# Kernel tuning notes

Hardware: AMD Instinct MI355X
Metric: run time of the kernel (lower is better)

## Reference

```python
import math
import jax, jax.numpy as jnp
import numpy as np
from jax import lax

B, C, O, K, WDIM, H, W = 8, 512, 512, 3, 512, 64, 64
CONV_SCALE = 1.0 / math.sqrt(C * K * K)
MOD_SCALE = 1.0 / math.sqrt(WDIM)


def setup_inputs() -> dict:
    key = jax.random.key(0)
    k1, k2, k3, k4 = jax.random.split(key, 4)
    return {
        "x": jax.random.normal(k1, (B, C, H, W), dtype=jnp.float32),
        "w": jax.random.normal(k2, (B, WDIM), dtype=jnp.float32),
        "base_weight": jax.random.normal(k3, (1, O, C, K, K), dtype=jnp.float32),
        "mod_weight": jax.random.normal(k4, (C, WDIM), dtype=jnp.float32),
        "mod_bias": jnp.zeros((C,), dtype=jnp.float32),
    }


def reference(x, w, base_weight, mod_weight, mod_bias):
    # EqualLinear modulation: s in (B, C), then +1
    s = w @ (mod_weight * MOD_SCALE).T + mod_bias + 1.0  # (B, C)
    # Per-sample modulated weights: (B, O, C, K, K)
    weight = CONV_SCALE * base_weight * s[:, None, :, None, None]
    # Demodulation
    d = lax.rsqrt(jnp.sum(weight * weight, axis=(2, 3, 4), keepdims=True))
    weight = weight * d
    pad = K // 2

    def conv_one(xi, wi):
        # xi: (C, H, W), wi: (O, C, K, K)
        return lax.conv_general_dilated(
            xi[None], wi, window_strides=(1, 1),
            padding=[(pad, pad), (pad, pad)],
            dimension_numbers=("NCHW", "OIHW", "NCHW"),
        )[0]

    return jax.vmap(conv_one)(x, weight)  # (B, O, H, W)
```

## Files before the change

### kernel.cpp

```cpp
#include <hip/hip_runtime.h>
#include <stdint.h>


#define MOD_SCALE  0.044194173824159216f
#define CONV_SCALE 0.014731391274719739f

typedef __attribute__((ext_vector_type(4))) float f32x4;
typedef __attribute__((ext_vector_type(8))) short bf16x8;

__device__ inline unsigned short f2bf(float f) {
  uint32_t u = __float_as_uint(f);
  uint32_t r = (u + 0x7fffu + ((u >> 16) & 1u)) >> 16;
  return (unsigned short)r;
}

__device__ inline void gload_lds16(const void* g, void* l) {
  __builtin_amdgcn_global_load_lds(
      (const __attribute__((address_space(1))) void*)g,
      (__attribute__((address_space(3))) void*)l, 16, 0, 0);
}

__global__ __launch_bounds__(256) void k_style(const float* __restrict__ w,
                                               const float* __restrict__ modw,
                                               const float* __restrict__ modb,
                                               float* __restrict__ s_out) {
  __shared__ float red[256];
  const int tid = threadIdx.x;
  const int sb = blockIdx.x;
  const int cb = sb & 7, b = sb >> 3;
  const int cl = tid >> 2, qq = tid & 3;
  const int c = (cb << 6) + cl;
  const float4* wd = (const float4*)(w + (b << 9) + (qq << 7));
  const float4* md = (const float4*)(modw + ((size_t)c << 9) + (qq << 7));
  float acc = 0.f;
#pragma unroll
  for (int i = 0; i < 32; ++i) {
    float4 a = wd[i], m = md[i];
    acc += a.x * m.x + a.y * m.y + a.z * m.z + a.w * m.w;
  }
  red[tid] = acc;
  __syncthreads();
  if (tid < 64) {
    float v = red[tid * 4] + red[tid * 4 + 1] + red[tid * 4 + 2] + red[tid * 4 + 3];
    int cc = (cb << 6) + tid;
    s_out[(b << 9) + cc] = v * MOD_SCALE + modb[cc] + 1.0f;
  }
}

__global__ __launch_bounds__(256) void k_prep(const float* __restrict__ x,
                                              const float* __restrict__ s,
                                              unsigned short* __restrict__ xp) {
  __shared__ uint32_t tb[64 * 260];
  const int blk = blockIdx.x;
  const int tid = threadIdx.x;
  if (blk < 512) {
    const int b = blk >> 6, y = blk & 63;
    const int px4 = tid & 15;
    const int cp  = tid >> 4;
    const float* xb = x + (size_t)(b << 9) * 4096 + (y << 6) + (px4 << 2);
    const float* sb = s + (b << 9);
#pragma unroll
    for (int it = 0; it < 16; ++it) {
      const int cpair = cp + (it << 4);
      const int c0 = cpair << 1;
      const float4 a0 = *(const float4*)(xb + (size_t)c0 * 4096);
      const float4 a1 = *(const float4*)(xb + (size_t)(c0 + 1) * 4096);
      const float s0 = sb[c0], s1 = sb[c0 + 1];
      const int pxb = px4 << 2;
      tb[(pxb + 0) * 260 + cpair] = (uint32_t)f2bf(a0.x * s0) | ((uint32_t)f2bf(a1.x * s1) << 16);
      tb[(pxb + 1) * 260 + cpair] = (uint32_t)f2bf(a0.y * s0) | ((uint32_t)f2bf(a1.y * s1) << 16);
      tb[(pxb + 2) * 260 + cpair] = (uint32_t)f2bf(a0.z * s0) | ((uint32_t)f2bf(a1.z * s1) << 16);
      tb[(pxb + 3) * 260 + cpair] = (uint32_t)f2bf(a0.w * s0) | ((uint32_t)f2bf(a1.w * s1) << 16);
    }
    __syncthreads();
    const int wv = tid >> 6, l = tid & 63;
    uint32_t* xpw = (uint32_t*)xp;
#pragma unroll
    for (int it = 0; it < 16; ++it) {
      const int px = (wv << 4) + it;
      const uint4 v = *(const uint4*)(tb + px * 260 + (l << 2));
      const size_t base = ((size_t)b * 4356 + (size_t)(y + 1) * 66 + (px + 1)) << 8;
      ((uint4*)(xpw + base))[l] = v;
    }
  } else {
    const int q = blk - 512;
    const int b = q / 260, p = q - b * 260;
    int py, px;
    if (p < 66)       { py = 0;       px = p; }
    else if (p < 132) { py = 65;      px = p - 66; }
    else if (p < 196) { py = p - 131; px = 0; }
    else              { py = p - 195; px = 65; }
    uint32_t* dst = (uint32_t*)(xp + ((size_t)b * 4356 + py * 66 + px) * 512);
    dst[tid] = 0u;
  }
}

__global__ __launch_bounds__(256) void k_fwd(const float* __restrict__ bw,
                                             const float* __restrict__ s,
                                             unsigned short* __restrict__ awT,
                                             float* __restrict__ d_out) {
  __shared__ float lw[4608];
  __shared__ float ls[4096];
  __shared__ float red[32];
  const int tid = threadIdx.x;
  const int o = blockIdx.x;
  {
    const float4* src = (const float4*)(bw + (size_t)o * 4608);
    float4* dst = (float4*)lw;
#pragma unroll
    for (int i = 0; i < 4; ++i) dst[tid + (i << 8)] = src[tid + (i << 8)];
    if (tid < 128) dst[tid + 1024] = src[tid + 1024];
  }
  {
    const float4* src = (const float4*)s;
    float4* dst = (float4*)ls;
#pragma unroll
    for (int i = 0; i < 4; ++i) dst[tid + (i << 8)] = src[tid + (i << 8)];
  }
  __syncthreads();
  const int c0 = tid << 1;
  const int base = c0 * 9;
  float wq0 = 0.f, wq1 = 0.f;
#pragma unroll
  for (int j = 0; j < 9; ++j) {
    float a = lw[base + j];      wq0 += a * a;
    float b2 = lw[base + 9 + j]; wq1 += b2 * b2;
  }
  const int lane = tid & 63, wv = tid >> 6;
#pragma unroll
  for (int b = 0; b < 8; ++b) {
    float s0 = ls[(b << 9) + c0], s1 = ls[(b << 9) + c0 + 1];
    float v = wq0 * s0 * s0 + wq1 * s1 * s1;
#pragma unroll
    for (int off = 32; off > 0; off >>= 1) v += __shfl_down(v, off, 64);
    if (lane == 0) red[(b << 2) + wv] = v;
  }
  __syncthreads();
  if (tid < 8) {
    float a = red[tid << 2] + red[(tid << 2) + 1] + red[(tid << 2) + 2] + red[(tid << 2) + 3];
    d_out[(tid << 9) + o] = rsqrtf(a * (1.0f / 4608.0f)) * CONV_SCALE;
  }
  uint32_t* dst = (uint32_t*)(awT + (size_t)o * 4608);
#pragma unroll
  for (int j = 0; j < 9; ++j)
    dst[(j << 8) + tid] = (uint32_t)f2bf(lw[base + j]) |
                          ((uint32_t)f2bf(lw[base + 9 + j]) << 16);
}

__global__ __launch_bounds__(256, 4) void k_conv(const unsigned short* __restrict__ awT,
                                                 const unsigned short* __restrict__ xpad,
                                                 const float* __restrict__ dmod,
                                                 float* __restrict__ out) {
  __shared__ alignas(16) unsigned short As[3 * 4096];
  __shared__ alignas(16) unsigned short Bs[4224];
  const int tid = threadIdx.x;
  const int b  = blockIdx.z;
  const int m0 = blockIdx.y << 7;
  const int n0 = blockIdx.x << 7;
  const int y0 = n0 >> 6;

  const int srow4 = tid >> 2;
  const int sl    = ((tid & 3) - (tid >> 3)) & 3;
  const int scol  = sl << 3;

  const unsigned short* A0 = awT + (size_t)(m0 + srow4) * 4608 + scol;
  const unsigned short* B0 = xpad + (size_t)b * (66 * 66 * 512)
                                  + (size_t)(y0 * 66 + srow4) * 512 + scol;

  const int lane = tid & 63;
  const int wv   = tid >> 6;
  const int moff = (wv >> 1) << 6;
  const int noff = (wv & 1) << 6;
  const int noffp = noff ? 66 : 0;
  const int lm   = lane & 15;
  const int g4   = lane >> 4;

  const int arow = moff + lm;
  const int aoff = arow * 32 + (((g4 + (arow >> 1)) & 3) << 3);
  int boff[3];
#pragma unroll
  for (int kx = 0; kx < 3; ++kx) {
    const int rb = noffp + lm + kx;
    boff[kx] = rb * 32 + (((g4 + (rb >> 1)) & 3) << 3);
  }

  f32x4 acc[4][4];
#pragma unroll
  for (int i = 0; i < 4; ++i)
#pragma unroll
    for (int j = 0; j < 4; ++j) acc[i][j] = (f32x4){0.f, 0.f, 0.f, 0.f};

#pragma unroll 1
  for (int ky = 0; ky < 3; ++ky) {
#pragma unroll 1
    for (int kb = 0; kb < 16; ++kb) {
      const int kcol = kb << 5;
#pragma unroll
      for (int kx = 0; kx < 3; ++kx) {
        const unsigned short* Ap = A0 + ((ky * 3 + kx) << 9) + kcol;
#pragma unroll
        for (int g = 0; g < 2; ++g)
          gload_lds16(Ap + (size_t)(g << 6) * 4608,
                      As + (kx << 12) + (((g << 8) + tid) << 3));
      }
      const unsigned short* Bp = B0 + (size_t)(ky * 66) * 512 + kcol;
#pragma unroll
      for (int g = 0; g < 2; ++g)
        gload_lds16(Bp + (size_t)(g << 6) * 512, Bs + (((g << 8) + tid) << 3));
      if (tid < 16) gload_lds16(Bp + (size_t)128 * 512, Bs + ((512 + tid) << 3));
      __syncthreads();
      __builtin_amdgcn_s_setprio(1);
#pragma unroll
      for (int kx = 0; kx < 3; ++kx) {
        bf16x8 af[4], bf[4];
        const unsigned short* pa = As + (kx << 12) + aoff;
        const unsigned short* pb = Bs + boff[kx];
#pragma unroll
        for (int i = 0; i < 4; ++i) af[i] = *(const bf16x8*)(pa + (i << 9));
#pragma unroll
        for (int j = 0; j < 4; ++j) bf[j] = *(const bf16x8*)(pb + (j << 9));
#pragma unroll
        for (int i = 0; i < 4; ++i)
#pragma unroll
          for (int j = 0; j < 4; ++j)
            acc[i][j] = __builtin_amdgcn_mfma_f32_16x16x32_bf16(af[i], bf[j], acc[i][j], 0, 0, 0);
      }
      __builtin_amdgcn_s_setprio(0);
      __syncthreads();
    }
  }

  const float* dB = dmod + (b << 9) + m0 + moff;
  float* op = out + (size_t)((b << 9) + m0 + moff) * 4096 + n0 + noff;
#pragma unroll
  for (int i = 0; i < 4; ++i) {
#pragma unroll
    for (int r = 0; r < 4; ++r) {
      const int m = i * 16 + (g4 << 2) + r;
      const float dm = dB[m];
#pragma unroll
      for (int j = 0; j < 4; ++j)
        op[(size_t)m * 4096 + (j << 4) + lm] = acc[i][j][r] * dm;
    }
  }
}

extern "C" void kernel_launch(void* const* d_in, const int* in_sizes, int n_in,
                              void* d_out, int out_size, void* d_ws, size_t ws_size,
                              hipStream_t stream) {
  const float* x    = (const float*)d_in[0];
  const float* w    = (const float*)d_in[1];
  const float* bw   = (const float*)d_in[2];
  const float* modw = (const float*)d_in[3];
  const float* modb = (const float*)d_in[4];
  float* out = (float*)d_out;
  char* ws = (char*)d_ws;

  float* s_buf = (float*)(ws);
  float* d_buf = (float*)(ws + 16384);
  unsigned short* awT  = (unsigned short*)(ws + 32768);
  unsigned short* xpad = (unsigned short*)(ws + 4751360);

  (void)in_sizes; (void)n_in; (void)out_size; (void)ws_size;

  k_style<<<64,   256, 0, stream>>>(w, modw, modb, s_buf);
  k_fwd  <<<512,  256, 0, stream>>>(bw, s_buf, awT, d_buf);
  k_prep <<<2592, 256, 0, stream>>>(x, s_buf, xpad);
  k_conv <<<dim3(32, 4, 8), 256, 0, stream>>>(awT, xpad, d_buf, out);
}
```

Measured before the change: 280.5 us.

## Enlarge conv tile to 128x256 and remap block index for L2 locality

```diff
diff --git a/kernel.cpp b/kernel.cpp
--- a/kernel.cpp
+++ b/kernel.cpp
@@ -147,48 +147,55 @@
                           ((uint32_t)f2bf(lw[base + 9 + j]) << 16);
 }
 
-__global__ __launch_bounds__(256, 4) void k_conv(const unsigned short* __restrict__ awT,
+__global__ __launch_bounds__(256, 2) void k_conv(const unsigned short* __restrict__ awT,
                                                  const unsigned short* __restrict__ xpad,
                                                  const float* __restrict__ dmod,
                                                  float* __restrict__ out) {
   __shared__ alignas(16) unsigned short As[3 * 4096];
-  __shared__ alignas(16) unsigned short Bs[4224];
-  const int tid = threadIdx.x;
-  const int b  = blockIdx.z;
-  const int m0 = blockIdx.y << 7;
-  const int n0 = blockIdx.x << 7;
-  const int y0 = n0 >> 6;
+  __shared__ alignas(16) unsigned short Bs[8448];
+  const int tid = threadIdx.x;
+
+  const int bid = blockIdx.x;
+  const int g   = bid & 7;
+  const int k   = bid >> 3;
+  const int nI  = k & 15;
+  const int zq  = k >> 4;
+  const int b   = (zq << 1) | (g >> 2);
+  const int m0  = (g & 3) << 7;
+  const int n0  = nI << 8;
+  const int y0  = nI << 2;
 
   const int srow4 = tid >> 2;
   const int sl    = ((tid & 3) - (tid >> 3)) & 3;
   const int scol  = sl << 3;
 
   const unsigned short* A0 = awT + (size_t)(m0 + srow4) * 4608 + scol;
-  const unsigned short* B0 = xpad + (size_t)b * (66 * 66 * 512)
-                                  + (size_t)(y0 * 66 + srow4) * 512 + scol;
+  const size_t bx = (size_t)b * (66 * 66 * 512);
+  const unsigned short* B0 = xpad + bx + (size_t)(y0 * 66 + srow4) * 512 + scol;
 
   const int lane = tid & 63;
   const int wv   = tid >> 6;
   const int moff = (wv >> 1) << 6;
-  const int noff = (wv & 1) << 6;
-  const int noffp = noff ? 66 : 0;
+  const int noff2 = (wv & 1) << 1;
   const int lm   = lane & 15;
   const int g4   = lane >> 4;
 
   const int arow = moff + lm;
   const int aoff = arow * 32 + (((g4 + (arow >> 1)) & 3) << 3);
-  int boff[3];
-#pragma unroll
-  for (int kx = 0; kx < 3; ++kx) {
-    const int rb = noffp + lm + kx;
-    boff[kx] = rb * 32 + (((g4 + (rb >> 1)) & 3) << 3);
-  }
-
-  f32x4 acc[4][4];
+  int boff[3][2];
+#pragma unroll
+  for (int kx = 0; kx < 3; ++kx)
+#pragma unroll
+    for (int jc = 0; jc < 2; ++jc) {
+      const int rb = (noff2 + jc) * 66 + lm + kx;
+      boff[kx][jc] = rb * 32 + (((g4 + (rb >> 1)) & 3) << 3);
+    }
+
+  f32x4 acc[4][8];
 #pragma unroll
   for (int i = 0; i < 4; ++i)
 #pragma unroll
-    for (int j = 0; j < 4; ++j) acc[i][j] = (f32x4){0.f, 0.f, 0.f, 0.f};
+    for (int j = 0; j < 8; ++j) acc[i][j] = (f32x4){0.f, 0.f, 0.f, 0.f};
 
 #pragma unroll 1
   for (int ky = 0; ky < 3; ++ky) {
@@ -199,31 +206,35 @@
       for (int kx = 0; kx < 3; ++kx) {
         const unsigned short* Ap = A0 + ((ky * 3 + kx) << 9) + kcol;
 #pragma unroll
-        for (int g = 0; g < 2; ++g)
-          gload_lds16(Ap + (size_t)(g << 6) * 4608,
-                      As + (kx << 12) + (((g << 8) + tid) << 3));
+        for (int g2 = 0; g2 < 2; ++g2)
+          gload_lds16(Ap + (size_t)(g2 << 6) * 4608,
+                      As + (kx << 12) + (((g2 << 8) + tid) << 3));
       }
       const unsigned short* Bp = B0 + (size_t)(ky * 66) * 512 + kcol;
 #pragma unroll
-      for (int g = 0; g < 2; ++g)
-        gload_lds16(Bp + (size_t)(g << 6) * 512, Bs + (((g << 8) + tid) << 3));
-      if (tid < 16) gload_lds16(Bp + (size_t)128 * 512, Bs + ((512 + tid) << 3));
+      for (int g2 = 0; g2 < 4; ++g2)
+        gload_lds16(Bp + (size_t)(g2 << 6) * 512, Bs + (((g2 << 8) + tid) << 3));
+      if (tid < 32) gload_lds16(Bp + (size_t)256 * 512, Bs + ((1024 + tid) << 3));
       __syncthreads();
       __builtin_amdgcn_s_setprio(1);
 #pragma unroll
       for (int kx = 0; kx < 3; ++kx) {
-        bf16x8 af[4], bf[4];
+        bf16x8 af[4], bfr[8];
         const unsigned short* pa = As + (kx << 12) + aoff;
-        const unsigned short* pb = Bs + boff[kx];
 #pragma unroll
         for (int i = 0; i < 4; ++i) af[i] = *(const bf16x8*)(pa + (i << 9));
-#pragma unroll
-        for (int j = 0; j < 4; ++j) bf[j] = *(const bf16x8*)(pb + (j << 9));
+        const unsigned short* pb0 = Bs + boff[kx][0];
+        const unsigned short* pb1 = Bs + boff[kx][1];
+#pragma unroll
+        for (int j = 0; j < 4; ++j) {
+          bfr[j]     = *(const bf16x8*)(pb0 + (j << 9));
+          bfr[4 + j] = *(const bf16x8*)(pb1 + (j << 9));
+        }
 #pragma unroll
         for (int i = 0; i < 4; ++i)
 #pragma unroll
-          for (int j = 0; j < 4; ++j)
-            acc[i][j] = __builtin_amdgcn_mfma_f32_16x16x32_bf16(af[i], bf[j], acc[i][j], 0, 0, 0);
+          for (int j = 0; j < 8; ++j)
+            acc[i][j] = __builtin_amdgcn_mfma_f32_16x16x32_bf16(af[i], bfr[j], acc[i][j], 0, 0, 0);
       }
       __builtin_amdgcn_s_setprio(0);
       __syncthreads();
@@ -231,7 +242,7 @@
   }
 
   const float* dB = dmod + (b << 9) + m0 + moff;
-  float* op = out + (size_t)((b << 9) + m0 + moff) * 4096 + n0 + noff;
+  float* op = out + (size_t)((b << 9) + m0 + moff) * 4096 + n0 + ((wv & 1) << 7);
 #pragma unroll
   for (int i = 0; i < 4; ++i) {
 #pragma unroll
@@ -239,7 +250,7 @@
       const int m = i * 16 + (g4 << 2) + r;
       const float dm = dB[m];
 #pragma unroll
-      for (int j = 0; j < 4; ++j)
+      for (int j = 0; j < 8; ++j)
         op[(size_t)m * 4096 + (j << 4) + lm] = acc[i][j][r] * dm;
     }
   }
@@ -266,5 +277,5 @@
   k_style<<<64,   256, 0, stream>>>(w, modw, modb, s_buf);
   k_fwd  <<<512,  256, 0, stream>>>(bw, s_buf, awT, d_buf);
   k_prep <<<2592, 256, 0, stream>>>(x, s_buf, xpad);
-  k_conv <<<dim3(32, 4, 8), 256, 0, stream>>>(awT, xpad, d_buf, out);
-}
+  k_conv <<<512,  256, 0, stream>>>(awT, xpad, d_buf, out);
+}
```

New measurement: 269.8 us. 1.04x faster.
